# Performance work log

Measured on AMD Instinct MI355X. Metric: run time of the kernel, lower is better.

The kernel has to match this reference:

```python
import jax, jax.numpy as jnp
import numpy as np

RATIO = 0.5  # SAGPooling default; k = ceil(ratio * N)


def setup_inputs() -> dict:
    key = jax.random.key(0)
    ks = jax.random.split(key, 6)
    N, D, E, DE = 100000, 128, 3200000, 16
    return {
        "x": jax.random.normal(ks[0], (N, D), dtype=jnp.float32),
        "score": jax.random.normal(ks[1], (N,), dtype=jnp.float32),
        "edge_index": jax.random.randint(ks[2], (2, E), 0, N, dtype=jnp.int64),
        "edge_attr": jax.random.normal(ks[3], (E, DE), dtype=jnp.float32),
        "node_type": jax.random.randint(ks[4], (N,), 0, 8, dtype=jnp.int64),
        "edge_lengths": jax.random.uniform(ks[5], (E,), dtype=jnp.float32),
    }


def reference(x, score, edge_index, edge_attr, node_type, edge_lengths):
    # Single-graph case (batch=None -> all-zeros batch), min_score=None branch.
    N = x.shape[0]
    k = int(np.ceil(RATIO * N))  # static top-k size

    # y = tanh(score); i = top_k(y); X' = (X * tanh(y))_i
    s = jnp.tanh(score)
    vals, perm = jax.lax.top_k(s, k)           # vals == s[perm], descending
    x_p = x[perm] * vals[:, None]              # [k, D]

    # filter_adj: relabel kept nodes 0..k-1, drop edges touching removed nodes.
    cluster = jnp.full((N,), -1, dtype=edge_index.dtype)
    cluster = cluster.at[perm].set(jnp.arange(k, dtype=edge_index.dtype))
    row = cluster[edge_index[0]]               # [E]
    col = cluster[edge_index[1]]               # [E]
    edge_mask = (row >= 0) & (col >= 0)        # valid-edge mask (padded form)

    # jit-friendly padded equivalent of torch's dynamic compaction:
    new_edge_index = jnp.stack([jnp.where(edge_mask, row, 0),
                                jnp.where(edge_mask, col, 0)], axis=0)
    edge_attr_p = jnp.where(edge_mask[:, None], edge_attr, 0.0)
    edge_lengths_p = jnp.where(edge_mask, edge_lengths, 0.0)

    return (x_p, new_edge_index, edge_attr_p, node_type[perm],
            perm, vals, edge_lengths_p, edge_mask)
```

## Files before the change

kernel.cpp:

```cpp
#include <hip/hip_runtime.h>
#include <math.h>

typedef unsigned int u32;
typedef unsigned long long u64;
typedef float f32x4 __attribute__((ext_vector_type(4)));

#define NDIG 2048
#define TILE 256
#define ROUNDS 4

__device__ __forceinline__ float xla_tanhf(float x) {
    float xc = fminf(fmaxf(x, -9.0f), 9.0f);
    float x2 = __fmul_rn(xc, xc);
    float p = -2.76076847742355e-16f;
    p = __fadd_rn(__fmul_rn(p, x2),  2.00018790482477e-13f);
    p = __fadd_rn(__fmul_rn(p, x2), -8.60467152213735e-11f);
    p = __fadd_rn(__fmul_rn(p, x2),  5.12229709037114e-08f);
    p = __fadd_rn(__fmul_rn(p, x2),  1.48572235717979e-05f);
    p = __fadd_rn(__fmul_rn(p, x2),  6.37261928875436e-04f);
    p = __fadd_rn(__fmul_rn(p, x2),  4.89352455891786e-03f);
    p = __fmul_rn(xc, p);
    float q = 1.19825839466702e-06f;
    q = __fadd_rn(__fmul_rn(q, x2),  1.18534705686654e-04f);
    q = __fadd_rn(__fmul_rn(q, x2),  2.26843463243900e-03f);
    q = __fadd_rn(__fmul_rn(q, x2),  4.89352518554385e-03f);
    float r = p / q;
    return (fabsf(x) < 0.0004f) ? x : r;
}

__device__ __forceinline__ u32 key_desc(float f) {
    u32 u = __float_as_uint(f);
    u = (u & 0x80000000u) ? ~u : (u | 0x80000000u);
    return ~u;
}

__global__ void k_countP(const float* __restrict__ score, u64* __restrict__ pack0,
                         int* __restrict__ cluster,
                         const int* __restrict__ ei, const int* __restrict__ ntype,
                         u32* __restrict__ flags, u32* __restrict__ hist_dt,
                         int N, int nT) {
    __shared__ u32 run[NDIG];
    const int tile = blockIdx.x;
    const int lane = threadIdx.x;
    if (tile == 0) {
        int v1 = ei[2 * lane + 1];
        u64 b1 = __ballot(v1 != 0);
        int v2 = ntype[2 * lane + 1];
        u64 b2 = __ballot(v2 != 0);
        if (lane == 0) { flags[0] = (b1 != 0ull) ? 1u : 0u;
                         flags[1] = (b2 != 0ull) ? 1u : 0u; }
    }
    for (int r = lane; r < NDIG; r += 64) run[r] = 0u;
    __syncthreads();
    const int base = tile * TILE;
    for (int j = 0; j < ROUNDS; ++j) {
        int e = base + j * 64 + lane;
        if (e < N) {
            float t = xla_tanhf(score[e]);
            cluster[e] = -1;
            u32 key = key_desc(t);
            pack0[e] = ((u64)key << 32) | (u32)e;
            u32 d = (key >> 10) & (NDIG - 1);
            u64 m = __ballot(1);
            for (int b = 0; b < 11; ++b) {
                u64 bb = __ballot((d >> b) & 1);
                m &= ((d >> b) & 1) ? bb : ~bb;
            }
            int leader = __ffsll(m) - 1;
            if (lane == leader) run[d] += (u32)__popcll(m);
        }
        __syncthreads();
    }
    for (int r = lane; r < NDIG; r += 64)
        hist_dt[(size_t)r * nT + tile] = run[r];
}

__global__ void k_count(const u64* __restrict__ src, u32* __restrict__ hist_dt,
                        int shift, int N, int nT) {
    __shared__ u32 run[NDIG];
    const int tile = blockIdx.x;
    const int lane = threadIdx.x;
    for (int r = lane; r < NDIG; r += 64) run[r] = 0u;
    __syncthreads();
    const int base = tile * TILE;
    for (int j = 0; j < ROUNDS; ++j) {
        int e = base + j * 64 + lane;
        if (e < N) {
            u32 key = (u32)(src[e] >> 32);
            u32 d = (key >> shift) & (NDIG - 1);
            u64 m = __ballot(1);
            for (int b = 0; b < 11; ++b) {
                u64 bb = __ballot((d >> b) & 1);
                m &= ((d >> b) & 1) ? bb : ~bb;
            }
            int leader = __ffsll(m) - 1;
            if (lane == leader) run[d] += (u32)__popcll(m);
        }
        __syncthreads();
    }
    for (int r = lane; r < NDIG; r += 64)
        hist_dt[(size_t)r * nT + tile] = run[r];
}

__global__ void k_red(const u32* __restrict__ h, u32* __restrict__ part) {
    __shared__ u32 sh[256];
    int b = blockIdx.x, t = threadIdx.x;
    sh[t] = h[(size_t)b * 256 + t];
    __syncthreads();
    for (int off = 128; off > 0; off >>= 1) {
        if (t < off) sh[t] += sh[t + off];
        __syncthreads();
    }
    if (t == 0) part[b] = sh[0];
}

__global__ void k_scn(u32* __restrict__ h, const u32* __restrict__ part) {
    __shared__ u32 sh[256];
    __shared__ u32 base_sh;
    int b = blockIdx.x, t = threadIdx.x;
    u32 acc = 0;
    for (int j = t; j < b; j += 256) acc += part[j];
    sh[t] = acc;
    __syncthreads();
    for (int off = 128; off > 0; off >>= 1) {
        if (t < off) sh[t] += sh[t + off];
        __syncthreads();
    }
    if (t == 0) base_sh = sh[0];
    __syncthreads();
    u32 base = base_sh;
    u32 v = h[(size_t)b * 256 + t];
    sh[t] = v;
    __syncthreads();
    for (int off = 1; off < 256; off <<= 1) {
        u32 x = sh[t];
        u32 y = (t >= off) ? sh[t - off] : 0u;
        __syncthreads();
        sh[t] = x + y;
        __syncthreads();
    }
    h[(size_t)b * 256 + t] = base + sh[t] - v;
}

__global__ void k_scatR(const u64* __restrict__ src, u64* __restrict__ dst,
                        const u32* __restrict__ scn, int shift, int N, int nT) {
    __shared__ u32 run[NDIG];
    const int tile = blockIdx.x;
    const int lane = threadIdx.x;
    for (int r = lane; r < NDIG; r += 64) run[r] = 0u;
    __syncthreads();
    const int base = tile * TILE;
    for (int j = 0; j < ROUNDS; ++j) {
        int e = base + j * 64 + lane;
        if (e < N) {
            u64 v = src[e];
            u32 key = (u32)(v >> 32);
            u32 d = (key >> shift) & (NDIG - 1);
            u64 m = __ballot(1);
            for (int b = 0; b < 11; ++b) {
                u64 bb = __ballot((d >> b) & 1);
                m &= ((d >> b) & 1) ? bb : ~bb;
            }
            u32 wrank = (u32)__popcll(m & ((1ull << lane) - 1ull));
            u32 old = run[d];
            u32 pos = scn[(size_t)d * nT + tile] + old + wrank;
            int leader = __ffsll(m) - 1;
            if (lane == leader) run[d] = old + (u32)__popcll(m);
            if (pos < (u32)N) dst[pos] = v;
        }
        __syncthreads();
    }
}

__global__ void k_pfix(const u64* __restrict__ srt, u64* __restrict__ pay64,
                       int* __restrict__ cluster,
                       const int* __restrict__ ntype, const u32* __restrict__ ntFlag,
                       float* __restrict__ o_nt, float* __restrict__ o_perm,
                       float* __restrict__ o_vals, int k, int N) {
    int r = blockIdx.x * blockDim.x + threadIdx.x;
    if (r >= N) return;
    u64 pk = srt[r];
    u64 t22 = pk >> 42;
    int rs = r;
    while (rs > 0 && (r - rs) < 4096 && (srt[rs - 1] >> 42) == t22) --rs;
    int rf = rs;
    for (int j = rs; j < N && (j - rs) < 8192; ++j) {
        u64 q = srt[j];
        if ((q >> 42) != t22) break;
        rf += (q < pk);
    }
    if (rf < k) {
        u32 ip = (u32)pk;
        if (ip >= (u32)N) ip = 0;
        u32 kb = (u32)(pk >> 32);
        u32 up = ~kb;
        u32 tb = (up >> 31) ? (up & 0x7FFFFFFFu) : ~up;
        pay64[rf] = ((u64)tb << 32) | ip;
        cluster[ip] = rf;
        o_perm[rf] = (float)ip;
        o_vals[rf] = __uint_as_float(tb);
        int nt = (*ntFlag == 0u) ? ntype[2 * (size_t)ip] : ntype[ip];
        o_nt[rf] = (float)nt;
    }
}

__global__ void k_gx(const u64* __restrict__ pay64,
                     const f32x4* __restrict__ x4, f32x4* __restrict__ out4,
                     int k, int Dv, int N) {
    int idx = blockIdx.x * blockDim.x + threadIdx.x;
    if (idx < k * Dv) {
        int r = idx / Dv, c = idx - r * Dv;
        u64 pv = pay64[r];
        u32 p = (u32)pv;
        float v = __uint_as_float((u32)(pv >> 32));
        if (p >= (u32)N) { p = 0; v = 0.0f; }
        f32x4 a = x4[(size_t)p * Dv + c];
        a = a * v;
        __builtin_nontemporal_store(a, out4 + idx);
    }
}

__global__ void k_ea(const int* __restrict__ ei, const u32* __restrict__ eiFlag,
                     const float* __restrict__ elen, const int* __restrict__ cluster,
                     const f32x4* __restrict__ attr4,
                     float* __restrict__ o_ei, float* __restrict__ o_len,
                     float* __restrict__ o_mask, f32x4* __restrict__ o_attr4,
                     int E, int N) {
    const bool w64 = (*eiFlag == 0u);
    const int lane = threadIdx.x & 63;
    const int waveId = (blockIdx.x * blockDim.x + threadIdx.x) >> 6;
    const int nWaves = (gridDim.x * blockDim.x) >> 6;
    const int nChunk = (E + 63) >> 6;
    for (int ch = waveId; ch < nChunk; ch += nWaves) {
        int e = ch * 64 + lane;
        int mfl = 0;
        if (e < E) {
            int a, b;
            if (w64) { a = ei[2 * (size_t)e]; b = ei[2 * ((size_t)E + (size_t)e)]; }
            else { a = ei[e]; b = ei[(size_t)E + e]; }
            bool ok = ((u32)a < (u32)N) && ((u32)b < (u32)N);
            int r  = ok ? cluster[a] : -1;
            int cc = ok ? cluster[b] : -1;
            bool m = (r >= 0) && (cc >= 0);
            mfl = m ? 1 : 0;
            __builtin_nontemporal_store(m ? (float)r  : 0.0f, o_ei + e);
            __builtin_nontemporal_store(m ? (float)cc : 0.0f, o_ei + (size_t)E + e);
            __builtin_nontemporal_store(m ? elen[e] : 0.0f, o_len + e);
            __builtin_nontemporal_store(m ? 1.0f : 0.0f, o_mask + e);
        }
        long long base4 = (long long)ch * 256;
        #pragma unroll
        for (int j = 0; j < 4; ++j) {
            long long idx4 = base4 + j * 64 + lane;
            int owner = j * 16 + (lane >> 2);
            int m = __shfl(mfl, owner);
            int ee = ch * 64 + owner;
            if (ee < E) {
                f32x4 v = {0.f, 0.f, 0.f, 0.f};
                if (m) v = attr4[idx4];
                __builtin_nontemporal_store(v, o_attr4 + idx4);
            }
        }
    }
}

extern "C" void kernel_launch(void* const* d_in, const int* in_sizes, int n_in,
                              void* d_out, int out_size, void* d_ws, size_t ws_size,
                              hipStream_t stream) {
    const float* x     = (const float*)d_in[0];
    const float* score = (const float*)d_in[1];
    const int*   ei    = (const int*)d_in[2];
    const float* eattr = (const float*)d_in[3];
    const int*   ntype = (const int*)d_in[4];
    const float* elen  = (const float*)d_in[5];

    const int N  = in_sizes[1];
    const int D  = in_sizes[0] / N;
    const int E  = in_sizes[5];
    const int DE = in_sizes[3] / E;
    const int k  = (N + 1) / 2;

    float* out = (float*)d_out;
    const size_t o_xp    = 0;
    const size_t o_ei    = o_xp    + (size_t)k * D;
    const size_t o_eattr = o_ei    + 2 * (size_t)E;
    const size_t o_nt    = o_eattr + (size_t)E * DE;
    const size_t o_perm  = o_nt    + (size_t)k;
    const size_t o_vals  = o_perm  + (size_t)k;
    const size_t o_elen  = o_vals  + (size_t)k;
    const size_t o_emask = o_elen  + (size_t)E;

    const int nT = (N + TILE - 1) / TILE;
    const int histN = NDIG * nT;
    const int nChunk = (histN + 255) / 256;

    char* ws = (char*)d_ws;
    u64* pack0   = (u64*)ws;     ws += 8 * (size_t)N;
    u64* pack1   = (u64*)ws;     ws += 8 * (size_t)N;
    u64* pay64   = (u64*)ws;     ws += 8 * (size_t)N;
    u32* hist_dt = (u32*)ws;     ws += 4 * (size_t)histN;
    u32* part    = (u32*)ws;     ws += 4 * (size_t)nChunk;
    u32* flags   = (u32*)ws;     ws += 4 * 2;
    int* cluster = (int*)ws;     ws += 4 * (size_t)N;

    const int nbN = (N + 255) / 256;

    k_countP<<<nT, 64, 0, stream>>>(score, pack0, cluster, ei, ntype, flags,
                                    hist_dt, N, nT);
    k_red<<<nChunk, 256, 0, stream>>>(hist_dt, part);
    k_scn<<<nChunk, 256, 0, stream>>>(hist_dt, part);
    k_scatR<<<nT, 64, 0, stream>>>(pack0, pack1, hist_dt, 10, N, nT);

    k_count<<<nT, 64, 0, stream>>>(pack1, hist_dt, 21, N, nT);
    k_red<<<nChunk, 256, 0, stream>>>(hist_dt, part);
    k_scn<<<nChunk, 256, 0, stream>>>(hist_dt, part);
    k_scatR<<<nT, 64, 0, stream>>>(pack1, pack0, hist_dt, 21, N, nT);

    k_pfix<<<nbN, 256, 0, stream>>>(pack0, pay64, cluster, ntype, &flags[1],
                                    out + o_nt, out + o_perm, out + o_vals, k, N);

    const int Dv = D / 4;
    const int gx = k * Dv;
    k_gx<<<(gx + 255) / 256, 256, 0, stream>>>(pay64, (const f32x4*)x,
                                               (f32x4*)(out + o_xp), k, Dv, N);
    k_ea<<<2048, 256, 0, stream>>>(ei, &flags[0], elen, cluster,
                                   (const f32x4*)eattr,
                                   out + o_ei, out + o_elen, out + o_emask,
                                   (f32x4*)(out + o_eattr), E, N);
}
```

Measured before the change: 135.5 us.

## Replace reduce-then-scan with single-pass decoupled look-back scan, enlarge radix tiles

The two-kernel reduce+scan over the digit histogram becomes one kernel. It uses a ticket-ordered decoupled look-back scan with per-block status flags, and the flags and tickets are zeroed inside the first count kernel. Radix sort tiles grow from 256 to 512 elements, which halves the number of tiles and the histogram size. This removes launches and the quadratic prefix-of-partials loop, at the cost of spin-waiting on global atomics and fewer blocks for the count and scatter kernels.

```diff
diff --git a/kernel.cpp b/kernel.cpp
--- a/kernel.cpp
+++ b/kernel.cpp
@@ -6,8 +6,8 @@
 typedef float f32x4 __attribute__((ext_vector_type(4)));
 
 #define NDIG 2048
-#define TILE 256
-#define ROUNDS 4
+#define TILE 512
+#define ROUNDS 8
 
 __device__ __forceinline__ float xla_tanhf(float x) {
     float xc = fminf(fmaxf(x, -9.0f), 9.0f);
@@ -38,15 +38,16 @@
                          int* __restrict__ cluster,
                          const int* __restrict__ ei, const int* __restrict__ ntype,
                          u32* __restrict__ flags, u32* __restrict__ hist_dt,
+                         u32* __restrict__ lbZero, int lbZeroN,
                          int N, int nT) {
     __shared__ u32 run[NDIG];
     const int tile = blockIdx.x;
     const int lane = threadIdx.x;
+    int gtid = tile * 64 + lane;
+    if (gtid < lbZeroN) lbZero[gtid] = 0u;
     if (tile == 0) {
-        int v1 = ei[2 * lane + 1];
-        u64 b1 = __ballot(v1 != 0);
-        int v2 = ntype[2 * lane + 1];
-        u64 b2 = __ballot(v2 != 0);
+        u64 b1 = __ballot(ei[2 * lane + 1] != 0);
+        u64 b2 = __ballot(ntype[2 * lane + 1] != 0);
         if (lane == 0) { flags[0] = (b1 != 0ull) ? 1u : 0u;
                          flags[1] = (b2 != 0ull) ? 1u : 0u; }
     }
@@ -102,44 +103,60 @@
         hist_dt[(size_t)r * nT + tile] = run[r];
 }
 
-__global__ void k_red(const u32* __restrict__ h, u32* __restrict__ part) {
+__global__ void k_scnL(u32* __restrict__ h, u32* __restrict__ flag,
+                       u32* __restrict__ ticket) {
     __shared__ u32 sh[256];
-    int b = blockIdx.x, t = threadIdx.x;
-    sh[t] = h[(size_t)b * 256 + t];
-    __syncthreads();
-    for (int off = 128; off > 0; off >>= 1) {
-        if (t < off) sh[t] += sh[t + off];
-        __syncthreads();
-    }
-    if (t == 0) part[b] = sh[0];
-}
-
-__global__ void k_scn(u32* __restrict__ h, const u32* __restrict__ part) {
-    __shared__ u32 sh[256];
-    __shared__ u32 base_sh;
-    int b = blockIdx.x, t = threadIdx.x;
-    u32 acc = 0;
-    for (int j = t; j < b; j += 256) acc += part[j];
-    sh[t] = acc;
-    __syncthreads();
-    for (int off = 128; off > 0; off >>= 1) {
-        if (t < off) sh[t] += sh[t + off];
-        __syncthreads();
-    }
-    if (t == 0) base_sh = sh[0];
-    __syncthreads();
-    u32 base = base_sh;
+    __shared__ u32 sBid, sExc;
+    const int t = threadIdx.x;
+    if (t == 0) { sBid = atomicAdd(ticket, 1u); sExc = 0u; }
+    __syncthreads();
+    const u32 b = sBid;
     u32 v = h[(size_t)b * 256 + t];
     sh[t] = v;
     __syncthreads();
     for (int off = 1; off < 256; off <<= 1) {
-        u32 x = sh[t];
-        u32 y = (t >= off) ? sh[t - off] : 0u;
+        u32 x = sh[t]; u32 y = (t >= off) ? sh[t - off] : 0u;
         __syncthreads();
         sh[t] = x + y;
         __syncthreads();
     }
-    h[(size_t)b * 256 + t] = base + sh[t] - v;
+    u32 incl = sh[t];
+    u32 agg  = sh[255];
+    if (t == 0) {
+        if (b == 0) atomicExch(&flag[0], (2u << 30) | agg);
+        else        atomicExch(&flag[b], (1u << 30) | agg);
+    }
+    __syncthreads();
+    if (b != 0) {
+        if (t < 64) {
+            u32 exc = 0;
+            int p = (int)b - 1;
+            for (;;) {
+                int idx = p - t;
+                u32 f = 0;
+                if (idx >= 0) { do { f = atomicOr(&flag[idx], 0u); } while ((f >> 30) == 0u); }
+                u32 st  = f >> 30;
+                u32 val = f & 0x3FFFFFFFu;
+                u64 m2 = __ballot(idx >= 0 && st == 2u);
+                if (m2 != 0ull) {
+                    int Ls = __ffsll((unsigned long long)m2) - 1;
+                    u32 c = (t <= Ls) ? val : 0u;
+                    for (int o = 32; o > 0; o >>= 1) c += __shfl_down(c, o);
+                    if (t == 0) sExc = exc + c;
+                    break;
+                } else {
+                    u32 c = (idx >= 0) ? val : 0u;
+                    for (int o = 32; o > 0; o >>= 1) c += __shfl_down(c, o);
+                    exc += __shfl(c, 0);
+                    p -= 64;
+                }
+            }
+        }
+        __syncthreads();
+        if (t == 0) atomicExch(&flag[b], (2u << 30) | (sExc + agg));
+    }
+    __syncthreads();
+    h[(size_t)b * 256 + t] = sExc + incl - v;
 }
 
 __global__ void k_scatR(const u64* __restrict__ src, u64* __restrict__ dst,
@@ -292,28 +309,29 @@
 
     const int nT = (N + TILE - 1) / TILE;
     const int histN = NDIG * nT;
-    const int nChunk = (histN + 255) / 256;
+    const int nB = histN / 256;
 
     char* ws = (char*)d_ws;
     u64* pack0   = (u64*)ws;     ws += 8 * (size_t)N;
     u64* pack1   = (u64*)ws;     ws += 8 * (size_t)N;
     u64* pay64   = (u64*)ws;     ws += 8 * (size_t)N;
     u32* hist_dt = (u32*)ws;     ws += 4 * (size_t)histN;
-    u32* part    = (u32*)ws;     ws += 4 * (size_t)nChunk;
+    u32* lbFlagA = (u32*)ws;     ws += 4 * (size_t)nB;
+    u32* lbFlagB = (u32*)ws;     ws += 4 * (size_t)nB;
+    u32* tickets = (u32*)ws;     ws += 4 * 2;
     u32* flags   = (u32*)ws;     ws += 4 * 2;
     int* cluster = (int*)ws;     ws += 4 * (size_t)N;
 
+    const int lbZeroN = 2 * nB + 2;
     const int nbN = (N + 255) / 256;
 
     k_countP<<<nT, 64, 0, stream>>>(score, pack0, cluster, ei, ntype, flags,
-                                    hist_dt, N, nT);
-    k_red<<<nChunk, 256, 0, stream>>>(hist_dt, part);
-    k_scn<<<nChunk, 256, 0, stream>>>(hist_dt, part);
+                                    hist_dt, lbFlagA, lbZeroN, N, nT);
+    k_scnL<<<nB, 256, 0, stream>>>(hist_dt, lbFlagA, &tickets[0]);
     k_scatR<<<nT, 64, 0, stream>>>(pack0, pack1, hist_dt, 10, N, nT);
 
     k_count<<<nT, 64, 0, stream>>>(pack1, hist_dt, 21, N, nT);
-    k_red<<<nChunk, 256, 0, stream>>>(hist_dt, part);
-    k_scn<<<nChunk, 256, 0, stream>>>(hist_dt, part);
+    k_scnL<<<nB, 256, 0, stream>>>(hist_dt, lbFlagB, &tickets[1]);
     k_scatR<<<nT, 64, 0, stream>>>(pack1, pack0, hist_dt, 21, N, nT);
 
     k_pfix<<<nbN, 256, 0, stream>>>(pack0, pay64, cluster, ntype, &flags[1],
```

Result: slower. 181.4 us (+33.9%).

## Enlarge radix-sort tiles to 1024 keys with 4-wave blocks and LDS atomics

Applied to the files above, without the earlier changes.

Radix sort tiles grow from 256 to 1024 elements and blocks from one wave to four, which cuts the number of per-tile histogram columns, and so the size of the scan, by four. Counting kernels swap the ballot-based match for shared-memory atomicAdd. The scatter kernel first builds per-wave digit counts and an exclusive prefix across waves, then ranks within each wave without per-round barriers, keeping the scatter stable. The cost is more LDS per block and atomic contention on repeated digits, and nChunk now assumes histN is a multiple of 256.

```diff
diff --git a/kernel.cpp b/kernel.cpp
--- a/kernel.cpp
+++ b/kernel.cpp
@@ -6,8 +6,8 @@
 typedef float f32x4 __attribute__((ext_vector_type(4)));
 
 #define NDIG 2048
-#define TILE 256
-#define ROUNDS 4
+#define TILE 1024
+#define NW 4
 
 __device__ __forceinline__ float xla_tanhf(float x) {
     float xc = fminf(fmaxf(x, -9.0f), 9.0f);
@@ -41,37 +41,29 @@
                          int N, int nT) {
     __shared__ u32 run[NDIG];
     const int tile = blockIdx.x;
-    const int lane = threadIdx.x;
-    if (tile == 0) {
-        int v1 = ei[2 * lane + 1];
-        u64 b1 = __ballot(v1 != 0);
-        int v2 = ntype[2 * lane + 1];
-        u64 b2 = __ballot(v2 != 0);
-        if (lane == 0) { flags[0] = (b1 != 0ull) ? 1u : 0u;
-                         flags[1] = (b2 != 0ull) ? 1u : 0u; }
-    }
-    for (int r = lane; r < NDIG; r += 64) run[r] = 0u;
+    const int tid = threadIdx.x;
+    if (tile == 0 && tid < 64) {
+        u64 b1 = __ballot(ei[2 * tid + 1] != 0);
+        u64 b2 = __ballot(ntype[2 * tid + 1] != 0);
+        if (tid == 0) { flags[0] = (b1 != 0ull) ? 1u : 0u;
+                        flags[1] = (b2 != 0ull) ? 1u : 0u; }
+    }
+    for (int r = tid; r < NDIG; r += 256) run[r] = 0u;
     __syncthreads();
     const int base = tile * TILE;
-    for (int j = 0; j < ROUNDS; ++j) {
-        int e = base + j * 64 + lane;
+    #pragma unroll
+    for (int j = 0; j < 4; ++j) {
+        int e = base + j * 256 + tid;
         if (e < N) {
             float t = xla_tanhf(score[e]);
             cluster[e] = -1;
             u32 key = key_desc(t);
             pack0[e] = ((u64)key << 32) | (u32)e;
-            u32 d = (key >> 10) & (NDIG - 1);
-            u64 m = __ballot(1);
-            for (int b = 0; b < 11; ++b) {
-                u64 bb = __ballot((d >> b) & 1);
-                m &= ((d >> b) & 1) ? bb : ~bb;
-            }
-            int leader = __ffsll(m) - 1;
-            if (lane == leader) run[d] += (u32)__popcll(m);
-        }
-        __syncthreads();
-    }
-    for (int r = lane; r < NDIG; r += 64)
+            atomicAdd(&run[(key >> 10) & (NDIG - 1)], 1u);
+        }
+    }
+    __syncthreads();
+    for (int r = tid; r < NDIG; r += 256)
         hist_dt[(size_t)r * nT + tile] = run[r];
 }
 
@@ -79,26 +71,20 @@
                         int shift, int N, int nT) {
     __shared__ u32 run[NDIG];
     const int tile = blockIdx.x;
-    const int lane = threadIdx.x;
-    for (int r = lane; r < NDIG; r += 64) run[r] = 0u;
+    const int tid = threadIdx.x;
+    for (int r = tid; r < NDIG; r += 256) run[r] = 0u;
     __syncthreads();
     const int base = tile * TILE;
-    for (int j = 0; j < ROUNDS; ++j) {
-        int e = base + j * 64 + lane;
+    #pragma unroll
+    for (int j = 0; j < 4; ++j) {
+        int e = base + j * 256 + tid;
         if (e < N) {
             u32 key = (u32)(src[e] >> 32);
-            u32 d = (key >> shift) & (NDIG - 1);
-            u64 m = __ballot(1);
-            for (int b = 0; b < 11; ++b) {
-                u64 bb = __ballot((d >> b) & 1);
-                m &= ((d >> b) & 1) ? bb : ~bb;
-            }
-            int leader = __ffsll(m) - 1;
-            if (lane == leader) run[d] += (u32)__popcll(m);
-        }
-        __syncthreads();
-    }
-    for (int r = lane; r < NDIG; r += 64)
+            atomicAdd(&run[(key >> shift) & (NDIG - 1)], 1u);
+        }
+    }
+    __syncthreads();
+    for (int r = tid; r < NDIG; r += 256)
         hist_dt[(size_t)r * nT + tile] = run[r];
 }
 
@@ -144,13 +130,33 @@
 
 __global__ void k_scatR(const u64* __restrict__ src, u64* __restrict__ dst,
                         const u32* __restrict__ scn, int shift, int N, int nT) {
-    __shared__ u32 run[NDIG];
+    __shared__ u32 wcur[NW][NDIG];
     const int tile = blockIdx.x;
-    const int lane = threadIdx.x;
-    for (int r = lane; r < NDIG; r += 64) run[r] = 0u;
-    __syncthreads();
-    const int base = tile * TILE;
-    for (int j = 0; j < ROUNDS; ++j) {
+    const int tid = threadIdx.x;
+    const int w = tid >> 6;
+    const int lane = tid & 63;
+    for (int r = tid; r < NW * NDIG; r += 256) ((u32*)wcur)[r] = 0u;
+    __syncthreads();
+    const int base = tile * TILE + w * 256;
+    #pragma unroll
+    for (int j = 0; j < 4; ++j) {
+        int e = base + j * 64 + lane;
+        if (e < N) {
+            u32 key = (u32)(src[e] >> 32);
+            atomicAdd(&wcur[w][(key >> shift) & (NDIG - 1)], 1u);
+        }
+    }
+    __syncthreads();
+    for (int r = tid; r < NDIG; r += 256) {
+        u32 a0 = wcur[0][r], a1 = wcur[1][r], a2 = wcur[2][r];
+        wcur[0][r] = 0u;
+        wcur[1][r] = a0;
+        wcur[2][r] = a0 + a1;
+        wcur[3][r] = a0 + a1 + a2;
+    }
+    __syncthreads();
+    #pragma unroll
+    for (int j = 0; j < 4; ++j) {
         int e = base + j * 64 + lane;
         if (e < N) {
             u64 v = src[e];
@@ -162,13 +168,12 @@
                 m &= ((d >> b) & 1) ? bb : ~bb;
             }
             u32 wrank = (u32)__popcll(m & ((1ull << lane) - 1ull));
-            u32 old = run[d];
+            u32 old = wcur[w][d];
             u32 pos = scn[(size_t)d * nT + tile] + old + wrank;
             int leader = __ffsll(m) - 1;
-            if (lane == leader) run[d] = old + (u32)__popcll(m);
+            if (lane == leader) wcur[w][d] = old + (u32)__popcll(m);
             if (pos < (u32)N) dst[pos] = v;
         }
-        __syncthreads();
     }
 }
 
@@ -292,7 +297,7 @@
 
     const int nT = (N + TILE - 1) / TILE;
     const int histN = NDIG * nT;
-    const int nChunk = (histN + 255) / 256;
+    const int nChunk = histN / 256;
 
     char* ws = (char*)d_ws;
     u64* pack0   = (u64*)ws;     ws += 8 * (size_t)N;
@@ -305,16 +310,16 @@
 
     const int nbN = (N + 255) / 256;
 
-    k_countP<<<nT, 64, 0, stream>>>(score, pack0, cluster, ei, ntype, flags,
-                                    hist_dt, N, nT);
+    k_countP<<<nT, 256, 0, stream>>>(score, pack0, cluster, ei, ntype, flags,
+                                     hist_dt, N, nT);
     k_red<<<nChunk, 256, 0, stream>>>(hist_dt, part);
     k_scn<<<nChunk, 256, 0, stream>>>(hist_dt, part);
-    k_scatR<<<nT, 64, 0, stream>>>(pack0, pack1, hist_dt, 10, N, nT);
-
-    k_count<<<nT, 64, 0, stream>>>(pack1, hist_dt, 21, N, nT);
+    k_scatR<<<nT, 256, 0, stream>>>(pack0, pack1, hist_dt, 10, N, nT);
+
+    k_count<<<nT, 256, 0, stream>>>(pack1, hist_dt, 21, N, nT);
     k_red<<<nChunk, 256, 0, stream>>>(hist_dt, part);
     k_scn<<<nChunk, 256, 0, stream>>>(hist_dt, part);
-    k_scatR<<<nT, 64, 0, stream>>>(pack1, pack0, hist_dt, 21, N, nT);
+    k_scatR<<<nT, 256, 0, stream>>>(pack1, pack0, hist_dt, 21, N, nT);
 
     k_pfix<<<nbN, 256, 0, stream>>>(pack0, pay64, cluster, ntype, &flags[1],
                                     out + o_nt, out + o_perm, out + o_vals, k, N);
```

After: 115.7 us (median of 2 runs). 14.6% less time.
